# Performance work log

Hardware: AMD Instinct MI355X
Metric: run time of the kernel (lower is better)

## Reference

```python
import jax, jax.numpy as jnp
import numpy as np

H, B = 128, 8          # hidden_channels, num_bilinear
NR, NS = 6, 7          # num_radial, num_spherical
E, T = 100000, 262144  # num_edges (rows of x), num_triplets


def _glorot(key, shape):
    fan = shape[-2] + shape[-1]
    return jax.random.normal(key, shape, jnp.float32) * jnp.sqrt(2.0 / fan)


def setup_inputs() -> dict:
    key = jax.random.key(0)
    ks = jax.random.split(key, 16)
    return {
        "x": jax.random.normal(ks[0], (E, H), jnp.float32),
        "radial_basis": jax.random.normal(ks[1], (E, NR), jnp.float32),
        "spherical_basis": jax.random.normal(ks[2], (T, NS * NR), jnp.float32),
        "edge_index_from": jax.random.randint(ks[3], (T,), 0, E, jnp.int32),
        "edge_index_to": jax.random.randint(ks[4], (T,), 0, E, jnp.int32),
        "w_rbf": _glorot(ks[5], (NR, H)),
        "w_sbf": _glorot(ks[6], (NS * NR, B)),
        "w_from": _glorot(ks[7], (H, H)),
        "b_from": jnp.zeros((H,), jnp.float32),
        "w_to": _glorot(ks[8], (H, H)),
        "b_to": jnp.zeros((H,), jnp.float32),
        "W": jax.random.normal(ks[9], (H, B, H), jnp.float32) * (2.0 / H),
        "rb_w": _glorot(ks[10], (1, 2, H, H)),
        "rb_b": jnp.zeros((1, 2, H), jnp.float32),
        "lin_w": _glorot(ks[11], (H, H)),
        "lin_b": jnp.zeros((H,), jnp.float32),
        "ra_w": _glorot(ks[12], (2, 2, H, H)),
        "ra_b": jnp.zeros((2, 2, H), jnp.float32),
    }


def _residual(h, w, b):
    # DimeNet ResidualLayer: h + act(lin2(act(lin1(h))))
    act = jax.nn.silu
    return h + act(act(h @ w[0] + b[0]) @ w[1] + b[1])


def reference(x, radial_basis, spherical_basis, edge_index_from, edge_index_to,
              w_rbf, w_sbf, w_from, b_from, w_to, b_to, W,
              rb_w, rb_b, lin_w, lin_b, ra_w, ra_b):
    act = jax.nn.silu
    rbf = radial_basis @ w_rbf                      # [E, H]
    sbf = spherical_basis @ w_sbf                   # [T, B]
    x_kj = act(x @ w_from + b_from) * rbf           # [E, H]
    gathered = x_kj[edge_index_from]                # [T, H] irregular gather
    # bilinear: out[w,i] = sum_{j,l} sbf[w,j] * gathered[w,l] * W[i,j,l]
    msg = jnp.einsum('wj,wl,ijl->wi', sbf, gathered, W, optimize=True)  # [T, H]
    agg = jax.ops.segment_sum(msg, edge_index_to, num_segments=x.shape[0])  # [E, H]
    x_ji = act(x @ w_to + b_to)
    h = x_ji + agg
    for i in range(rb_w.shape[0]):
        h = _residual(h, rb_w[i], rb_b[i])
    h = act(h @ lin_w + lin_b) + x
    for i in range(ra_w.shape[0]):
        h = _residual(h, ra_w[i], ra_b[i])
    return h
```

## Files before the change

### kernel.cpp

```cpp
#include <hip/hip_runtime.h>
#include <cstdint>


#define H 128
#define NB 8
#define NR 6
#define SBC 42
#define LDA 136
#define WFRAG 16384

using f16x8 = __attribute__((ext_vector_type(8))) _Float16;
using f32x4 = __attribute__((ext_vector_type(4))) float;

__device__ __forceinline__ float silu_f(float v){
  return v / (1.f + __expf(-v));
}
__device__ __forceinline__ f16x8 pack8(float4 a, float4 b){
  f16x8 h;
  h[0]=(_Float16)a.x; h[1]=(_Float16)a.y; h[2]=(_Float16)a.z; h[3]=(_Float16)a.w;
  h[4]=(_Float16)b.x; h[5]=(_Float16)b.y; h[6]=(_Float16)b.z; h[7]=(_Float16)b.w;
  return h;
}
__device__ __forceinline__ void lds_dma16(const void* g, void* l){
  __builtin_amdgcn_global_load_lds(
      (const __attribute__((address_space(1))) unsigned int*)g,
      (__attribute__((address_space(3))) unsigned int*)l, 16, 0, 0);
}
__device__ __forceinline__ void atomic_pk_add_f16(_Float16* addr, float lo, float hi){
  union { _Float16 h[2]; unsigned u; } d;
  d.h[0] = (_Float16)lo; d.h[1] = (_Float16)hi;
  asm volatile("global_atomic_pk_add_f16 %0, %1, off"
               :: "v"(addr), "v"(d.u) : "memory");
}

__global__ void prep_kernel(const float* __restrict__ w_from,
                            const float* __restrict__ w_to,
                            const float* __restrict__ rb_w,
                            const float* __restrict__ lin_w,
                            const float* __restrict__ ra_w,
                            const float* __restrict__ Wb,
                            _Float16* __restrict__ wf,
                            _Float16* __restrict__ Wf)
{
  int idx = blockIdx.x*256 + threadIdx.x;
  if (blockIdx.x < 72){
    int m = idx >> 11, c = idx & 2047;
    int nt = c >> 8, kk = (c>>6)&3, l = c&63, q = l>>4, l15 = l&15;
    const float* src;
    switch(m){
      case 0: src = w_from;       break;
      case 1: src = w_to;         break;
      case 2: src = rb_w;         break;
      case 3: src = rb_w + 16384; break;
      case 4: src = lin_w;        break;
      case 5: src = ra_w;         break;
      case 6: src = ra_w + 16384; break;
      case 7: src = ra_w + 32768; break;
      default: src = ra_w + 49152; break;
    }
    const float* p = src + (size_t)(kk*32 + q*8)*H + nt*16 + l15;
    f16x8 o;
    #pragma unroll
    for (int j=0;j<8;j++) o[j] = (_Float16)p[(size_t)j*H];
    *reinterpret_cast<f16x8*>(wf + (size_t)m*WFRAG + c*8) = o;
  } else {
    int t = idx - 72*256;
    int j = t >> 11, c = t & 2047;
    int nt = c >> 8, kk = (c>>6)&3, l = c&63, q = l>>4, l15 = l&15;
    const float4* p = reinterpret_cast<const float4*>(
        Wb + ((size_t)(nt*16+l15)*NB + j)*H + kk*32 + q*8);
    *reinterpret_cast<f16x8*>(Wf + (size_t)j*WFRAG + c*8) = pack8(p[0], p[1]);
  }
}

__global__ __launch_bounds__(256,2) void edge_kernel(
    const float* __restrict__ x,
    const float* __restrict__ radial,
    const float* __restrict__ w_rbf,
    const _Float16* __restrict__ wf,
    const float* __restrict__ b_from,
    const float* __restrict__ b_to,
    _Float16* __restrict__ x_kj, _Float16* __restrict__ agg, int E)
{
  __shared__ alignas(16) _Float16 sA[64*LDA];
  __shared__ alignas(16) _Float16 sO[64*LDA];
  __shared__ alignas(16) _Float16 sW[WFRAG];
  __shared__ float sRad[64*8];
  __shared__ float sWr[128*8];
  __shared__ float sBf[128];
  __shared__ float sBt[128];
  int tid = threadIdx.x;
  int e0 = blockIdx.x*64;
  int wave = tid>>6, lane = tid&63, l15 = lane&15, q = lane>>4;

  {
    const _Float16* gs = wf + (size_t)(wave*64 + lane)*8;
    _Float16* ls = sW + (size_t)wave*512;
    #pragma unroll
    for (int u=0;u<8;u++) lds_dma16(gs + (size_t)u*2048, ls + (size_t)u*2048);
  }
  {
    int row = tid>>2, cs = (tid&3)*32;
    bool ok = (e0+row) < E;
    const float4* src = reinterpret_cast<const float4*>(x + (size_t)(e0+row)*H + cs);
    #pragma unroll
    for (int i=0;i<4;i++){
      float4 u0{0,0,0,0}, u1{0,0,0,0};
      if (ok){ u0 = src[2*i]; u1 = src[2*i+1]; }
      *reinterpret_cast<f16x8*>(&sA[row*LDA + cs + i*8]) = pack8(u0,u1);
    }
  }
  for (int i=tid; i<64*NR; i+=256){
    int r=i/NR, c=i%NR;
    sRad[r*8+c] = (e0+r < E) ? radial[(size_t)(e0+r)*NR + c] : 0.f;
  }
  for (int i=tid; i<NR*H; i+=256){
    int c=i>>7, n=i&127;
    sWr[n*8+c] = w_rbf[i];
  }
  if (tid < H){ sBf[tid] = b_from[tid]; sBt[tid] = b_to[tid]; }
  __syncthreads();

  f32x4 acc[8];
  auto gemm = [&](){
    #pragma unroll
    for (int nt=0;nt<8;nt++) acc[nt] = f32x4{0.f,0.f,0.f,0.f};
    int ar = (wave*16 + l15)*LDA;
    #pragma unroll
    for (int kk=0;kk<4;kk++){
      f16x8 a = *reinterpret_cast<const f16x8*>(&sA[ar + kk*32 + q*8]);
      #pragma unroll
      for (int nt=0;nt<8;nt++){
        f16x8 b = *reinterpret_cast<const f16x8*>(&sW[((nt*4+kk)*64 + lane)*8]);
        acc[nt] = __builtin_amdgcn_mfma_f32_16x16x32_f16(a, b, acc[nt], 0,0,0);
      }
    }
  };

  gemm();
  __syncthreads();
  {
    const _Float16* gs = wf + WFRAG + (size_t)(wave*64 + lane)*8;
    _Float16* ls = sW + (size_t)wave*512;
    #pragma unroll
    for (int u=0;u<8;u++) lds_dma16(gs + (size_t)u*2048, ls + (size_t)u*2048);
  }
  #pragma unroll
  for (int nt=0;nt<8;nt++)
    #pragma unroll
    for (int r=0;r<4;r++){
      int rl = wave*16 + q*4 + r, col = nt*16 + l15;
      float v = silu_f(acc[nt][r] + sBf[col]);
      float rb = 0.f;
      #pragma unroll
      for (int c=0;c<NR;c++) rb += sRad[rl*8+c]*sWr[col*8+c];
      sO[rl*LDA+col] = (_Float16)(v*rb);
    }
  {
    int row=tid>>2, cs=(tid&3)*32;
    if (e0+row < E)
      #pragma unroll
      for (int i=0;i<4;i++)
        *reinterpret_cast<f16x8*>(x_kj + (size_t)(e0+row)*H + cs + i*8) =
          *reinterpret_cast<const f16x8*>(&sO[row*LDA + cs + i*8]);
  }
  __syncthreads();
  gemm();
  #pragma unroll
  for (int nt=0;nt<8;nt++)
    #pragma unroll
    for (int r=0;r<4;r++){
      int rl = wave*16 + q*4 + r, col = nt*16 + l15;
      sO[rl*LDA+col] = (_Float16)silu_f(acc[nt][r] + sBt[col]);
    }
  {
    int row=tid>>2, cs=(tid&3)*32;
    if (e0+row < E)
      #pragma unroll
      for (int i=0;i<4;i++)
        *reinterpret_cast<f16x8*>(agg + (size_t)(e0+row)*H + cs + i*8) =
          *reinterpret_cast<const f16x8*>(&sO[row*LDA + cs + i*8]);
  }
}

__global__ __launch_bounds__(256,3) void bilinear_kernel(
    const _Float16* __restrict__ x_kj,
    const float* __restrict__ sph,
    const float* __restrict__ w_sbf,
    const _Float16* __restrict__ Wf,
    const int* __restrict__ e_from, const int* __restrict__ e_to,
    _Float16* __restrict__ agg)
{
  __shared__ alignas(16) _Float16 wch[WFRAG];
  __shared__ float ssb[128*NB];
  __shared__ float sw[SBC*NB];
  __shared__ int sdst[128];
  int tid = threadIdx.x;
  long long t0 = (long long)blockIdx.x * 128;
  int wave = tid>>6, lane = tid&63, l15 = lane&15, q = lane>>4;
  int m0 = wave*32;

  int ef0 = e_from[t0 + m0 + l15];
  int ef1 = e_from[t0 + m0 + 16 + l15];
  f16x8 aR0[4], aR1[4];
  #pragma unroll
  for (int kk=0;kk<4;kk++){
    aR0[kk] = *reinterpret_cast<const f16x8*>(x_kj + (size_t)ef0*H + kk*32 + q*8);
    aR1[kk] = *reinterpret_cast<const f16x8*>(x_kj + (size_t)ef1*H + kk*32 + q*8);
  }

  {
    float4* scr = reinterpret_cast<float4*>(wch);
    const float4* g = reinterpret_cast<const float4*>(sph + t0*SBC);
    for (int i=tid; i<128*SBC/4; i+=256) scr[i] = g[i];
  }
  for (int i=tid; i<SBC*NB; i+=256) sw[i] = w_sbf[i];
  if (tid < 128) sdst[tid] = e_to[t0 + tid];
  __syncthreads();
  {
    int row = tid>>1, half = tid&1;
    const float* srow = reinterpret_cast<const float*>(wch) + row*SBC;
    float a4[4] = {0.f,0.f,0.f,0.f};
    for (int c=0;c<SBC;c++){
      float v = srow[c];
      #pragma unroll
      for (int cc=0;cc<4;cc++) a4[cc] += v * sw[c*NB + half*4 + cc];
    }
    #pragma unroll
    for (int cc=0;cc<4;cc++) ssb[row*NB + half*4 + cc] = a4[cc];
  }

  f32x4 acc[2][8];
  #pragma unroll
  for (int mt=0;mt<2;mt++)
    #pragma unroll
    for (int nt=0;nt<8;nt++) acc[mt][nt] = f32x4{0.f,0.f,0.f,0.f};

  for (int jj=0;jj<NB;jj++){
    __syncthreads();
    {
      const _Float16* gs = Wf + (size_t)jj*WFRAG + (size_t)(wave*64 + lane)*8;
      _Float16* ls = wch + (size_t)(wave*64)*8;
      #pragma unroll
      for (int u=0;u<8;u++)
        lds_dma16(gs + (size_t)u*2048, ls + (size_t)u*2048);
    }
    __syncthreads();
    _Float16 s0 = (_Float16)ssb[(m0+l15)*NB + jj];
    _Float16 s1 = (_Float16)ssb[(m0+16+l15)*NB + jj];
    #pragma unroll
    for (int kk=0;kk<4;kk++){
      f16x8 a0 = aR0[kk] * s0;
      f16x8 a1 = aR1[kk] * s1;
      #pragma unroll
      for (int nt=0;nt<8;nt++){
        f16x8 b = *reinterpret_cast<const f16x8*>(&wch[((nt*4+kk)*64 + lane)*8]);
        acc[0][nt] = __builtin_amdgcn_mfma_f32_16x16x32_f16(a0, b, acc[0][nt], 0,0,0);
        acc[1][nt] = __builtin_amdgcn_mfma_f32_16x16x32_f16(a1, b, acc[1][nt], 0,0,0);
      }
    }
  }

  int odd = l15 & 1;
  #pragma unroll
  for (int mt=0;mt<2;mt++)
    #pragma unroll
    for (int ntp=0;ntp<4;ntp++)
      #pragma unroll
      for (int r=0;r<4;r++){
        float a = acc[mt][2*ntp  ][r];
        float b = acc[mt][2*ntp+1][r];
        float ax = __shfl_xor(a, 1);
        float bx = __shfl_xor(b, 1);
        int rl  = m0 + mt*16 + q*4 + r;
        int col = 32*ntp + (odd ? 15 + l15 : l15);
        atomic_pk_add_f16(agg + (size_t)sdst[rl]*H + col,
                          odd ? bx : a, odd ? b : ax);
      }
}

__global__ __launch_bounds__(256,3) void post_kernel(
    const float* __restrict__ x, const _Float16* __restrict__ agg,
    const _Float16* __restrict__ wf,
    const float* __restrict__ rb_b, const float* __restrict__ lin_b,
    const float* __restrict__ ra_b,
    float* __restrict__ out, int E)
{
  __shared__ alignas(16) _Float16 sIn[64*LDA];
  __shared__ alignas(16) _Float16 sW[WFRAG];
  int tid = threadIdx.x, e0 = blockIdx.x*64;
  int wave = tid>>6, lane = tid&63, l15 = lane&15, q = lane>>4;

  const float* bptr[7] = {rb_b, rb_b+128, lin_b, ra_b, ra_b+128, ra_b+256, ra_b+384};

  {
    int row=tid>>2, cs=(tid&3)*32;
    bool ok = (e0+row) < E;
    f16x8 z;
    #pragma unroll
    for (int j=0;j<8;j++) z[j] = (_Float16)0.f;
    #pragma unroll
    for (int i=0;i<4;i++){
      f16x8 v = z;
      if (ok) v = *reinterpret_cast<const f16x8*>(agg + (size_t)(e0+row)*H + cs + i*8);
      *reinterpret_cast<f16x8*>(&sIn[row*LDA + cs + i*8]) = v;
    }
  }
  float h[8][4];
  #pragma unroll
  for (int nt=0;nt<8;nt++)
    #pragma unroll
    for (int r=0;r<4;r++)
      h[nt][r] = (float)sIn[(wave*16+q*4+r)*LDA + nt*16 + l15];

  f32x4 acc[8];
  #pragma unroll
  for (int s=0;s<7;s++){
    if (s > 0) __syncthreads();
    {
      const _Float16* gs = wf + (size_t)(s+2)*WFRAG + (size_t)(wave*64 + lane)*8;
      _Float16* ls = sW + (size_t)wave*512;
      #pragma unroll
      for (int u=0;u<8;u++) lds_dma16(gs + (size_t)u*2048, ls + (size_t)u*2048);
    }
    float bcol[8];
    #pragma unroll
    for (int nt=0;nt<8;nt++) bcol[nt] = bptr[s][nt*16 + l15];
    #pragma unroll
    for (int nt=0;nt<8;nt++) acc[nt] = f32x4{0.f,0.f,0.f,0.f};
    __syncthreads();
    int ar = (wave*16 + l15)*LDA;
    #pragma unroll
    for (int kk=0;kk<4;kk++){
      f16x8 a = *reinterpret_cast<const f16x8*>(&sIn[ar + kk*32 + q*8]);
      #pragma unroll
      for (int nt=0;nt<8;nt++){
        f16x8 b = *reinterpret_cast<const f16x8*>(&sW[((nt*4+kk)*64 + lane)*8]);
        acc[nt] = __builtin_amdgcn_mfma_f32_16x16x32_f16(a, b, acc[nt], 0,0,0);
      }
    }
    #pragma unroll
    for (int nt=0;nt<8;nt++)
      #pragma unroll
      for (int r=0;r<4;r++){
        int rl = wave*16 + q*4 + r, col = nt*16 + l15;
        float v = silu_f(acc[nt][r] + bcol[nt]);
        if (s==0 || s==3 || s==5){
          sIn[rl*LDA+col] = (_Float16)v;
        } else if (s==1 || s==4){
          h[nt][r] += v;
          sIn[rl*LDA+col] = (_Float16)h[nt][r];
        } else if (s==2){
          bool ok = (e0+rl) < E;
          float xv = ok ? x[(size_t)(e0+rl)*H + col] : 0.f;
          h[nt][r] = v + xv;
          sIn[rl*LDA+col] = (_Float16)h[nt][r];
        } else {
          h[nt][r] += v;
          if ((e0+rl) < E) out[(size_t)(e0+rl)*H + col] = h[nt][r];
        }
      }
  }
}

extern "C" void kernel_launch(void* const* d_in, const int* in_sizes, int n_in,
                              void* d_out, int out_size, void* d_ws, size_t ws_size,
                              hipStream_t stream)
{
  const float* x      = (const float*)d_in[0];
  const float* radial = (const float*)d_in[1];
  const float* sph    = (const float*)d_in[2];
  const int* e_from   = (const int*)d_in[3];
  const int* e_to     = (const int*)d_in[4];
  const float* w_rbf  = (const float*)d_in[5];
  const float* w_sbf  = (const float*)d_in[6];
  const float* w_from = (const float*)d_in[7];
  const float* b_from = (const float*)d_in[8];
  const float* w_to   = (const float*)d_in[9];
  const float* b_to   = (const float*)d_in[10];
  const float* Wb     = (const float*)d_in[11];
  const float* rb_w   = (const float*)d_in[12];
  const float* rb_b   = (const float*)d_in[13];
  const float* lin_w  = (const float*)d_in[14];
  const float* lin_b  = (const float*)d_in[15];
  const float* ra_w   = (const float*)d_in[16];
  const float* ra_b   = (const float*)d_in[17];

  int E = in_sizes[0] / H;
  int T = in_sizes[3];

  char* ws = (char*)d_ws;
  _Float16* aggh = (_Float16*)ws;
  _Float16* wf   = (_Float16*)(ws + (size_t)E*H*2);
  _Float16* Wf   = wf + 9*WFRAG;
  _Float16* x_kj = (_Float16*)d_out;

  prep_kernel<<<136, 256, 0, stream>>>(w_from, w_to, rb_w, lin_w, ra_w, Wb, wf, Wf);
  edge_kernel<<<(E+63)/64, 256, 0, stream>>>(x, radial, w_rbf, wf, b_from, b_to,
                                             x_kj, aggh, E);
  bilinear_kernel<<<T/128, 256, 0, stream>>>(x_kj, sph, w_sbf, Wf, e_from, e_to, aggh);
  post_kernel<<<(E+63)/64, 256, 0, stream>>>(x, aggh, wf, rb_b, lin_b, ra_b,
                                             (float*)d_out, E);
}
```

Measured before the change: 383.0 us.

## Double-buffer weight staging in half-tiles to overlap LDS DMA with MFMA

```diff
diff --git a/kernel.cpp b/kernel.cpp
--- a/kernel.cpp
+++ b/kernel.cpp
@@ -229,6 +229,17 @@
     #pragma unroll
     for (int cc=0;cc<4;cc++) ssb[row*NB + half*4 + cc] = a4[cc];
   }
+  __syncthreads();
+
+  auto stage_phase = [&](int pp){
+    int jn = pp>>1, hn = pp&1;
+    const _Float16* gs = Wf + (size_t)jn*WFRAG + (size_t)hn*8192
+                            + (size_t)wave*2048 + (size_t)lane*8;
+    _Float16* ls = wch + (size_t)hn*8192 + (size_t)wave*2048;
+    #pragma unroll
+    for (int u=0;u<4;u++)
+      lds_dma16(gs + (size_t)u*512, ls + (size_t)u*512);
+  };
 
   f32x4 acc[2][8];
   #pragma unroll
@@ -236,29 +247,31 @@
     #pragma unroll
     for (int nt=0;nt<8;nt++) acc[mt][nt] = f32x4{0.f,0.f,0.f,0.f};
 
-  for (int jj=0;jj<NB;jj++){
-    __syncthreads();
-    {
-      const _Float16* gs = Wf + (size_t)jj*WFRAG + (size_t)(wave*64 + lane)*8;
-      _Float16* ls = wch + (size_t)(wave*64)*8;
-      #pragma unroll
-      for (int u=0;u<8;u++)
-        lds_dma16(gs + (size_t)u*2048, ls + (size_t)u*2048);
-    }
-    __syncthreads();
-    _Float16 s0 = (_Float16)ssb[(m0+l15)*NB + jj];
-    _Float16 s1 = (_Float16)ssb[(m0+16+l15)*NB + jj];
+  stage_phase(0);
+  __syncthreads();
+
+  _Float16 s0 = (_Float16)0.f, s1 = (_Float16)0.f;
+  #pragma unroll
+  for (int p=0;p<16;p++){
+    const int jj = p>>1, h = p&1;
+    if (p < 15) stage_phase(p+1);
+    if (h == 0){
+      s0 = (_Float16)ssb[(m0+l15)*NB + jj];
+      s1 = (_Float16)ssb[(m0+16+l15)*NB + jj];
+    }
+    const _Float16* cur = wch + h*8192;
     #pragma unroll
     for (int kk=0;kk<4;kk++){
       f16x8 a0 = aR0[kk] * s0;
       f16x8 a1 = aR1[kk] * s1;
       #pragma unroll
-      for (int nt=0;nt<8;nt++){
-        f16x8 b = *reinterpret_cast<const f16x8*>(&wch[((nt*4+kk)*64 + lane)*8]);
-        acc[0][nt] = __builtin_amdgcn_mfma_f32_16x16x32_f16(a0, b, acc[0][nt], 0,0,0);
-        acc[1][nt] = __builtin_amdgcn_mfma_f32_16x16x32_f16(a1, b, acc[1][nt], 0,0,0);
+      for (int ntl=0;ntl<4;ntl++){
+        f16x8 b = *reinterpret_cast<const f16x8*>(&cur[(ntl*4+kk)*512 + lane*8]);
+        acc[0][h*4+ntl] = __builtin_amdgcn_mfma_f32_16x16x32_f16(a0, b, acc[0][h*4+ntl], 0,0,0);
+        acc[1][h*4+ntl] = __builtin_amdgcn_mfma_f32_16x16x32_f16(a1, b, acc[1][h*4+ntl], 0,0,0);
       }
     }
+    if (p < 15) __syncthreads();
   }
 
   int odd = l15 & 1;
@@ -293,6 +306,18 @@
 
   const float* bptr[7] = {rb_b, rb_b+128, lin_b, ra_b, ra_b+128, ra_b+256, ra_b+384};
 
+  auto stage_phase = [&](int pp){
+    int sn = pp>>1, hn = pp&1;
+    const _Float16* gs = wf + (size_t)(sn+2)*WFRAG + (size_t)hn*8192
+                            + (size_t)wave*2048 + (size_t)lane*8;
+    _Float16* ls = sW + (size_t)hn*8192 + (size_t)wave*2048;
+    #pragma unroll
+    for (int u=0;u<4;u++)
+      lds_dma16(gs + (size_t)u*512, ls + (size_t)u*512);
+  };
+
+  stage_phase(0);
+
   {
     int row=tid>>2, cs=(tid&3)*32;
     bool ok = (e0+row) < E;
@@ -312,54 +337,58 @@
     #pragma unroll
     for (int r=0;r<4;r++)
       h[nt][r] = (float)sIn[(wave*16+q*4+r)*LDA + nt*16 + l15];
+  __syncthreads();
 
   f32x4 acc[8];
-  #pragma unroll
-  for (int s=0;s<7;s++){
-    if (s > 0) __syncthreads();
-    {
-      const _Float16* gs = wf + (size_t)(s+2)*WFRAG + (size_t)(wave*64 + lane)*8;
-      _Float16* ls = sW + (size_t)wave*512;
-      #pragma unroll
-      for (int u=0;u<8;u++) lds_dma16(gs + (size_t)u*2048, ls + (size_t)u*2048);
-    }
-    float bcol[8];
-    #pragma unroll
-    for (int nt=0;nt<8;nt++) bcol[nt] = bptr[s][nt*16 + l15];
-    #pragma unroll
-    for (int nt=0;nt<8;nt++) acc[nt] = f32x4{0.f,0.f,0.f,0.f};
-    __syncthreads();
-    int ar = (wave*16 + l15)*LDA;
+  float bcol[8];
+  f16x8 af[4];
+  int ar = (wave*16 + l15)*LDA;
+  #pragma unroll
+  for (int p=0;p<14;p++){
+    const int s = p>>1, hf = p&1;
+    if (p < 13) stage_phase(p+1);
+    if (hf == 0){
+      #pragma unroll
+      for (int nt=0;nt<8;nt++) acc[nt] = f32x4{0.f,0.f,0.f,0.f};
+      #pragma unroll
+      for (int nt=0;nt<8;nt++) bcol[nt] = bptr[s][nt*16 + l15];
+      #pragma unroll
+      for (int kk=0;kk<4;kk++)
+        af[kk] = *reinterpret_cast<const f16x8*>(&sIn[ar + kk*32 + q*8]);
+    }
+    const _Float16* cur = sW + hf*8192;
     #pragma unroll
     for (int kk=0;kk<4;kk++){
-      f16x8 a = *reinterpret_cast<const f16x8*>(&sIn[ar + kk*32 + q*8]);
-      #pragma unroll
-      for (int nt=0;nt<8;nt++){
-        f16x8 b = *reinterpret_cast<const f16x8*>(&sW[((nt*4+kk)*64 + lane)*8]);
-        acc[nt] = __builtin_amdgcn_mfma_f32_16x16x32_f16(a, b, acc[nt], 0,0,0);
+      #pragma unroll
+      for (int ntl=0;ntl<4;ntl++){
+        f16x8 b = *reinterpret_cast<const f16x8*>(&cur[(ntl*4+kk)*512 + lane*8]);
+        acc[hf*4+ntl] = __builtin_amdgcn_mfma_f32_16x16x32_f16(af[kk], b, acc[hf*4+ntl], 0,0,0);
       }
     }
-    #pragma unroll
-    for (int nt=0;nt<8;nt++)
-      #pragma unroll
-      for (int r=0;r<4;r++){
-        int rl = wave*16 + q*4 + r, col = nt*16 + l15;
-        float v = silu_f(acc[nt][r] + bcol[nt]);
-        if (s==0 || s==3 || s==5){
-          sIn[rl*LDA+col] = (_Float16)v;
-        } else if (s==1 || s==4){
-          h[nt][r] += v;
-          sIn[rl*LDA+col] = (_Float16)h[nt][r];
-        } else if (s==2){
-          bool ok = (e0+rl) < E;
-          float xv = ok ? x[(size_t)(e0+rl)*H + col] : 0.f;
-          h[nt][r] = v + xv;
-          sIn[rl*LDA+col] = (_Float16)h[nt][r];
-        } else {
-          h[nt][r] += v;
-          if ((e0+rl) < E) out[(size_t)(e0+rl)*H + col] = h[nt][r];
+    if (hf == 1){
+      #pragma unroll
+      for (int nt=0;nt<8;nt++)
+        #pragma unroll
+        for (int r=0;r<4;r++){
+          int rl = wave*16 + q*4 + r, col = nt*16 + l15;
+          float v = silu_f(acc[nt][r] + bcol[nt]);
+          if (s==0 || s==3 || s==5){
+            sIn[rl*LDA+col] = (_Float16)v;
+          } else if (s==1 || s==4){
+            h[nt][r] += v;
+            sIn[rl*LDA+col] = (_Float16)h[nt][r];
+          } else if (s==2){
+            bool ok = (e0+rl) < E;
+            float xv = ok ? x[(size_t)(e0+rl)*H + col] : 0.f;
+            h[nt][r] = v + xv;
+            sIn[rl*LDA+col] = (_Float16)h[nt][r];
+          } else {
+            h[nt][r] += v;
+            if ((e0+rl) < E) out[(size_t)(e0+rl)*H + col] = h[nt][r];
+          }
         }
-      }
+    }
+    if (p < 13) __syncthreads();
   }
 }
 
```

New measurement: 413.2 us. 7.9% more time.
